# Performance work log

Measured on AMD Instinct MI355X. Metric: run time of the kernel, lower is better.

Reference implementation:

```python
import jax, jax.numpy as jnp
import numpy as np

B, S, N, E = 16, 2048, 256, 4096      # batch, tokens, max entities, edges per sample
H, LD, ETR = 512, 16, 768             # hidden_size, label_emb_dim, transformer dim
D = H + LD                            # graph_dim = 528
C1 = 3                                # num_edge_classes + 1
GL = 2                                # gcn_layers
NLBL = 15                             # num_node_classes + 2


def setup_inputs() -> dict:
    key = jax.random.key(0)
    ks = jax.random.split(key, 14)
    s = 0.02
    inp = {}
    inp["emb"] = jax.random.normal(ks[0], (B, S, ETR), jnp.float32)
    inp["ent_indices"] = jax.random.randint(ks[1], (B, S), 0, N + 1)
    inp["ent_labels"] = jax.random.randint(ks[2], (B, N), 0, NLBL)
    inp["edge_index"] = jax.random.randint(ks[3], (B, 2, E), 0, N + 1)
    inp["edge_attr"] = jax.random.randint(ks[4], (B, E), 0, C1)
    inp["cands"] = jax.random.randint(ks[5], (B, N + 1, N + 1), 0, 2).astype(bool)
    inp["W_red"] = jax.random.normal(ks[6], (ETR, H), jnp.float32) * s
    inp["b_red"] = jnp.zeros((H,), jnp.float32)
    inp["emb_label_tbl"] = jax.random.normal(ks[7], (NLBL, LD), jnp.float32) * s
    inp["W_gcn"] = jax.random.normal(ks[8], (C1, GL, D, D), jnp.float32) * s
    inp["b_gcn"] = jnp.zeros((C1, GL, D), jnp.float32)
    inp["W_head"] = jax.random.normal(ks[9], (D, D), jnp.float32) * s
    inp["b_head"] = jnp.zeros((D,), jnp.float32)
    inp["W_tail"] = jax.random.normal(ks[10], (D, D), jnp.float32) * s
    inp["b_tail"] = jnp.zeros((D,), jnp.float32)
    inp["W_out"] = jax.random.normal(ks[11], (D, C1), jnp.float32) * s
    inp["b_out"] = jnp.zeros((C1,), jnp.float32)
    return inp


def _gcn_layer(x, src, dst, w_e, W, b):
    """PyG GCNConv with edge weights w_e (0/1 relation mask) and self loops.
    x: [n, D]; src/dst: [E]; aggregation flow source->target."""
    n = x.shape[0]
    h = x @ W
    deg = jax.ops.segment_sum(w_e, dst, num_segments=n) + 1.0  # +1 self loop
    dinv = jax.lax.rsqrt(deg)
    coef = w_e * dinv[src] * dinv[dst]                         # D^-1/2 A D^-1/2
    agg = jax.ops.segment_sum(coef[:, None] * h[src], dst, num_segments=n)
    return agg + h / deg[:, None] + b                          # self-loop norm = 1/deg


def reference(emb, ent_indices, ent_labels, edge_index, edge_attr, cands,
              W_red, b_red, emb_label_tbl, W_gcn, b_gcn,
              W_head, b_head, W_tail, b_tail, W_out, b_out):
    n_nodes = cands.shape[1]  # max_num_ent + 1
    # fc_reduction of frozen transformer embeddings
    red = emb @ W_red + b_red                                   # [B,S,H]
    # tag-based segment aggregation: max over (mask * emb) == max(segment_max, 0)
    seg_max = jax.vmap(lambda e, ids: jax.ops.segment_max(e, ids, num_segments=n_nodes))(red, ent_indices)
    ent_hidden = jnp.maximum(seg_max, 0.0).at[:, 0, :].set(0.0)  # tag 0 stays zero
    # label embeddings: tag t uses ent_labels[:, t-1]; zeroed where label==0
    lab = emb_label_tbl[ent_labels] * (ent_labels != 0)[..., None].astype(red.dtype)
    lab0 = jnp.broadcast_to(emb_label_tbl[0], (lab.shape[0], 1, lab.shape[-1]))
    label_part = jnp.concatenate([lab0, lab], axis=1)           # [B,n_nodes,LD]
    x0 = jnp.concatenate([label_part, ent_hidden], axis=-1)     # [B,n_nodes,D]
    # multi-relation GCN: per edge class, stacked GCNConv, summed then averaged
    src, dst = edge_index[:, 0], edge_index[:, 1]
    layer_v = jax.vmap(_gcn_layer, in_axes=(0, 0, 0, 0, None, None))
    result = jnp.zeros_like(x0)
    n_cls = W_gcn.shape[0]
    for c in range(n_cls):
        w_e = (edge_attr == c).astype(x0.dtype)
        x = x0
        for l in range(W_gcn.shape[1]):
            x = layer_v(x, src, dst, w_e, W_gcn[c, l], b_gcn[c, l])
        result = result + x
    result = result / n_cls
    # head/tail projections and 'add' pairwise features gated by candidate mask
    x_head = result @ W_head + b_head
    x_tail = result @ W_tail + b_tail
    m = cands[:, :, 1:].astype(x0.dtype)                        # [B,n_nodes,n_nodes-1]
    # fc_out is linear: ((h_i + t_j) * m_ij) @ W + b == m_ij*(hW_i + tW_j) + b
    hW = x_head @ W_out                                         # [B,n_nodes,C1]
    tW = x_tail[:, 1:] @ W_out                                  # [B,n_nodes-1,C1]
    logits = (hW[:, :, None, :] + tW[:, None, :, :]) * m[..., None] + b_out
    return logits  # [B, n_nodes, n_nodes-1, C1] edge-class logits
```

## Files before the change

kernel.cpp:

```cpp
#include <hip/hip_runtime.h>
#include <hip/hip_bf16.h>

typedef unsigned short u16;
typedef __attribute__((ext_vector_type(8))) short short8;
typedef __attribute__((ext_vector_type(4))) float floatx4;

#define B_ 16
#define S_ 2048
#define NNODE 257
#define E_ 4096
#define ETR_ 768
#define H_ 512
#define D_ 528
#define KPAD 544
#define NC 3
#define NROW (B_*NNODE)
#define DD (D_*D_)

#define BM 128
#define BN 128
#define BK 32

__device__ inline u16 f2b(float x) {
    __hip_bfloat16 h = __float2bfloat16(x);
    return *(u16*)&h;
}
__device__ inline float b2f(u16 u) {
    return __uint_as_float(((unsigned)u) << 16);
}

__device__ inline void gll16(const u16* g, u16* l) {
    __builtin_amdgcn_global_load_lds(
        (const __attribute__((address_space(1))) void*)g,
        (__attribute__((address_space(3))) void*)l,
        16, 0, 0);
}

__device__ inline int clampi(int v, int hi) { return v < hi ? v : hi; }

__global__ void cvt_bf16(const float* __restrict__ in, u16* __restrict__ out, int n4)
{
    const int i = blockIdx.x * 256 + threadIdx.x;
    if (i < n4) {
        const float4 f = ((const float4*)in)[i];
        ushort4 o;
        o.x = f2b(f.x); o.y = f2b(f.y); o.z = f2b(f.z); o.w = f2b(f.w);
        ((ushort4*)out)[i] = o;
    }
}

__global__ void transpose_cvt(const float* __restrict__ in, u16* __restrict__ out,
                              int R, int Cc, size_t instride, size_t outstride,
                              int opitch)
{
    __shared__ float t[32][33];
    const int z = blockIdx.z;
    const int tx = threadIdx.x & 31, ty = threadIdx.x >> 5;
    const int c0 = blockIdx.x * 32, r0 = blockIdx.y * 32;
    const float* ip = in + z * instride;
    u16* op = out + z * outstride;
#pragma unroll
    for (int i = 0; i < 4; i++) {
        const int r = r0 + ty + i * 8, c = c0 + tx;
        if (r < R && c < Cc) t[ty + i * 8][tx] = ip[(size_t)r * Cc + c];
    }
    __syncthreads();
#pragma unroll
    for (int i = 0; i < 4; i++) {
        const int c = c0 + ty + i * 8, r = r0 + tx;
        if (c < Cc && r < R) op[(size_t)c * opitch + r] = f2b(t[tx][ty + i * 8]);
    }
}

template<int SWZ, int OB16>
__global__ __launch_bounds__(256)
void gemm_mfma(const u16* __restrict__ A, const u16* __restrict__ Wt,
               const float* __restrict__ bias_base, size_t bias_stride,
               void* __restrict__ Cv, int M, int N, int K, float scale,
               size_t astride, size_t wstride, size_t cstride, int cpitch)
{
    __shared__ u16 SS[8192];
    const int tid = threadIdx.x;
    const int wave = tid >> 6, lane = tid & 63;
    const int quad = lane >> 4, l16 = lane & 15;
    const int z = blockIdx.z;
    int bx = blockIdx.x, by = blockIdx.y;
    if (SWZ) {
        const int lin = blockIdx.x + (blockIdx.y << 2);
        bx = (lin >> 3) & 3;
        by = (lin & 7) + ((lin >> 5) << 3);
    }
    const int m0 = by * BM, n0 = bx * BN;

    floatx4 acc[2][8];
#pragma unroll
    for (int t = 0; t < 2; t++)
#pragma unroll
        for (int u = 0; u < 8; u++)
#pragma unroll
            for (int r = 0; r < 4; r++) acc[t][u][r] = 0.f;

    const int srow = tid >> 2;
    const int scol = (((tid & 3) ^ ((srow >> 1) & 3))) * 8;
    const u16* aP0 = A + z * astride + (size_t)clampi(m0 + srow,      M - 1) * K + scol;
    const u16* aP1 = A + z * astride + (size_t)clampi(m0 + 64 + srow, M - 1) * K + scol;
    const u16* bP0 = Wt + z * wstride + (size_t)clampi(n0 + srow,      N - 1) * K + scol;
    const u16* bP1 = Wt + z * wstride + (size_t)clampi(n0 + 64 + srow, N - 1) * K + scol;
    u16* const ls = &SS[0] + wave * 512;

    const int sw8 = ((l16 >> 1) & 3) * 8;

    for (int k0 = 0; k0 < K; k0 += BK) {
        gll16(aP0 + k0, ls);
        gll16(aP1 + k0, ls + 2048);
        gll16(bP0 + k0, ls + 4096);
        gll16(bP1 + k0, ls + 6144);
        __syncthreads();
        short8 af[2], bfv[8];
        af[0] = *(const short8*)&SS[(wave * 32 + l16) * 32 + ((quad * 8) ^ sw8)];
        af[1] = *(const short8*)&SS[(wave * 32 + 16 + l16) * 32 + ((quad * 8) ^ sw8)];
#pragma unroll
        for (int u = 0; u < 8; u++)
            bfv[u] = *(const short8*)&SS[4096 + (u * 16 + l16) * 32 + ((quad * 8) ^ sw8)];
#pragma unroll
        for (int t = 0; t < 2; t++)
#pragma unroll
            for (int u = 0; u < 8; u++)
                acc[t][u] = __builtin_amdgcn_mfma_f32_16x16x32_bf16(af[t], bfv[u], acc[t][u], 0, 0, 0);
        __syncthreads();
    }

    const float* bias = bias_base ? (bias_base + z * bias_stride) : nullptr;
#pragma unroll
    for (int t = 0; t < 2; t++) {
#pragma unroll
        for (int r = 0; r < 4; r++) {
            const int m = m0 + wave * 32 + t * 16 + quad * 4 + r;
            if (m >= M) continue;
#pragma unroll
            for (int u = 0; u < 8; u++) {
                const int n = n0 + u * 16 + l16;
                if (n < N) {
                    const float v = acc[t][u][r] * scale + (bias ? bias[n] : 0.f);
                    if (OB16) {
                        u16* Cb = (u16*)Cv;
                        Cb[z * cstride + (size_t)m * cpitch + n] = f2b(v);
                    } else {
                        float* Cf = (float*)Cv;
                        Cf[z * cstride + (size_t)m * cpitch + n] = v;
                    }
                }
            }
        }
    }
}

template<int MODE>
__global__ __launch_bounds__(256)
void gemm64(const float* __restrict__ A, const float* __restrict__ W,
            const float* __restrict__ bias, float* __restrict__ C,
            int M, int N, int K, float scale,
            const int* __restrict__ segidx, float* __restrict__ segout)
{
    __shared__ float Asl[16][68];
    __shared__ float Bsl[16][64];
    const int tid = threadIdx.x;
    const int tx = tid & 15, ty = tid >> 4;
    const int m0 = blockIdx.y * 64, n0 = blockIdx.x * 64;
    const int arow = tid >> 2, acol = (tid & 3) * 4;
    const int brow = tid >> 4, bcol = (tid & 15) * 4;

    float acc[4][4];
#pragma unroll
    for (int i = 0; i < 4; i++)
#pragma unroll
        for (int j = 0; j < 4; j++) acc[i][j] = 0.f;

    for (int kk = 0; kk < K; kk += 16) {
        float4 av = make_float4(0.f, 0.f, 0.f, 0.f);
        if (m0 + arow < M) av = *(const float4*)(A + (size_t)(m0 + arow) * K + kk + acol);
        Asl[acol + 0][arow] = av.x; Asl[acol + 1][arow] = av.y;
        Asl[acol + 2][arow] = av.z; Asl[acol + 3][arow] = av.w;
        float4 bv = make_float4(0.f, 0.f, 0.f, 0.f);
        if (n0 + bcol < N) bv = *(const float4*)(W + (size_t)(kk + brow) * N + n0 + bcol);
        *(float4*)&Bsl[brow][bcol] = bv;
        __syncthreads();
#pragma unroll
        for (int k = 0; k < 16; k++) {
            const float4 a = *(const float4*)&Asl[k][ty * 4];
            const float4 b = *(const float4*)&Bsl[k][tx * 4];
            const float af[4] = { a.x, a.y, a.z, a.w };
            const float bfv[4] = { b.x, b.y, b.z, b.w };
#pragma unroll
            for (int i = 0; i < 4; i++)
#pragma unroll
                for (int j = 0; j < 4; j++) acc[i][j] += af[i] * bfv[j];
        }
        __syncthreads();
    }

#pragma unroll
    for (int i = 0; i < 4; i++) {
        const int m = m0 + ty * 4 + i;
        if (m >= M) continue;
        if (MODE == 1) {
            const int bb = m >> 11;
            const int idx = segidx[m];
            float* const srow = segout + (((size_t)bb * NNODE + idx) << 9);
#pragma unroll
            for (int j = 0; j < 4; j++) {
                const int n = n0 + tx * 4 + j;
                const float v = acc[i][j] + (bias ? bias[n] : 0.f);
                atomicMax(((int*)srow) + n, __float_as_int(v));
            }
        } else {
#pragma unroll
            for (int j = 0; j < 4; j++) {
                const int n = n0 + tx * 4 + j;
                if (n < N) {
                    const float v = acc[i][j] * scale + (bias ? bias[n] : 0.f);
                    C[(size_t)m * N + n] = v;
                }
            }
        }
    }
}

__global__ void csr_all(const int* __restrict__ ent_indices,
                        int* __restrict__ rptr, int* __restrict__ rlist,
                        const int* __restrict__ edge_index, const int* __restrict__ edge_attr,
                        float* __restrict__ degf, int* __restrict__ csr_ptr,
                        int2* __restrict__ csr_sc)
{
    __shared__ int cnt[NC * NNODE];
    __shared__ float dinvl[NC * NNODE];
    const int b = blockIdx.x;
    const int tid = threadIdx.x;

    const int* idx = ent_indices + (size_t)b * S_;
    for (int i = tid; i < NNODE; i += 256) cnt[i] = 0;
    __syncthreads();
    for (int r = tid; r < S_; r += 256) atomicAdd(&cnt[idx[r]], 1);
    __syncthreads();
    if (tid == 0) {
        int run = 0;
        for (int i = 0; i < NNODE; i++) { const int c = cnt[i]; cnt[i] = run; run += c; }
    }
    __syncthreads();
    for (int i = tid; i < NNODE; i += 256) rptr[b * (NNODE + 1) + i] = cnt[i];
    if (tid == 0) rptr[b * (NNODE + 1) + NNODE] = S_;
    __syncthreads();
    for (int r = tid; r < S_; r += 256) {
        const int pos = atomicAdd(&cnt[idx[r]], 1);
        rlist[(size_t)b * S_ + pos] = r;
    }
    __syncthreads();

    const int* src = edge_index + (size_t)b * 2 * E_;
    const int* dst = src + E_;
    const int* attr = edge_attr + (size_t)b * E_;
    for (int i = tid; i < NC * NNODE; i += 256) cnt[i] = 0;
    __syncthreads();
    for (int e = tid; e < E_; e += 256) atomicAdd(&cnt[attr[e] * NNODE + dst[e]], 1);
    __syncthreads();
    for (int i = tid; i < NC * NNODE; i += 256) {
        const float d = (float)cnt[i] + 1.0f;
        degf[(size_t)b * NC * NNODE + i] = d;
        dinvl[i] = rsqrtf(d);
    }
    __syncthreads();
    if (tid == 0) {
        int run = 0;
        for (int i = 0; i < NC * NNODE; i++) { const int c = cnt[i]; cnt[i] = run; run += c; }
    }
    __syncthreads();
    for (int i = tid; i < NC * NNODE; i += 256) csr_ptr[(size_t)b * NC * NNODE + i] = cnt[i];
    __syncthreads();
    for (int e = tid; e < E_; e += 256) {
        const int a = attr[e], d = dst[e], s = src[e];
        const int pos = atomicAdd(&cnt[a * NNODE + d], 1);
        const float cf = dinvl[a * NNODE + s] * dinvl[a * NNODE + d];
        csr_sc[(size_t)b * E_ + pos] = make_int2(s, __float_as_int(cf));
    }
}

__global__ __launch_bounds__(256)
void segmax_x0(const u16* __restrict__ redC, const int* __restrict__ rptr,
               const int* __restrict__ rlist, const float* __restrict__ b_red,
               const int* __restrict__ ent_labels, const float* __restrict__ tbl,
               u16* __restrict__ x0b)
{
    const int bn = blockIdx.x;
    const int b = bn / NNODE, n = bn % NNODE;
    const int tid = threadIdx.x;
    const int c0 = tid * 2;
    const int start = rptr[b * (NNODE + 1) + n];
    const int end   = (n == 0) ? start : rptr[b * (NNODE + 1) + n + 1];
    float m0 = -INFINITY, m1 = -INFINITY;
    const int* rl = rlist + (size_t)b * S_;
    for (int i = start; i < end; i++) {
        const u16* row = redC + ((size_t)b * S_ + rl[i]) * H_;
        const unsigned v = *(const unsigned*)(row + c0);
        m0 = fmaxf(m0, __uint_as_float((v & 0xffffu) << 16));
        m1 = fmaxf(m1, __uint_as_float(v & 0xffff0000u));
    }
    float h0, h1;
    if (n == 0) { h0 = 0.f; h1 = 0.f; }
    else {
        h0 = fmaxf(m0 + b_red[c0], 0.f);
        h1 = fmaxf(m1 + b_red[c0 + 1], 0.f);
    }
    u16* orow = x0b + (size_t)bn * KPAD;
    *(unsigned*)(orow + 16 + c0) = (unsigned)f2b(h0) | ((unsigned)f2b(h1) << 16);
    if (tid < 16) {
        float v;
        if (n == 0) v = tbl[tid];
        else {
            const int lab = ent_labels[b * (NNODE - 1) + (n - 1)];
            v = (lab != 0) ? tbl[lab * 16 + tid] : 0.f;
        }
        orow[tid] = f2b(v);
    } else if (tid < 32) {
        orow[512 + tid] = 0;
    }
}

template<int OUTB>
__global__ void build_x0(const float* __restrict__ seg, const int* __restrict__ ent_labels,
                         const float* __restrict__ tbl, float* __restrict__ x0f,
                         u16* __restrict__ x0b)
{
    const int bn = blockIdx.x;
    const int b = bn / NNODE, n = bn % NNODE;
    const int CMAX = OUTB ? KPAD : D_;
    for (int col = threadIdx.x; col < CMAX; col += blockDim.x) {
        float v;
        if (col >= D_) {
            v = 0.f;
        } else if (col < 16) {
            if (n == 0) v = tbl[col];
            else {
                const int lab = ent_labels[b * (NNODE - 1) + (n - 1)];
                v = (lab != 0) ? tbl[lab * 16 + col] : 0.f;
            }
        } else {
            v = (n == 0) ? 0.f : seg[(((size_t)b * NNODE + n) << 9) + (col - 16)];
        }
        if (OUTB) x0b[(size_t)bn * KPAD + col] = f2b(v);
        else      x0f[(size_t)bn * D_ + col] = v;
    }
}

template<int OUT>
__global__ __launch_bounds__(256)
void gcn_gather(const float* __restrict__ h, size_t hstride,
                const float* __restrict__ degf,
                const int* __restrict__ csr_ptr, const int2* __restrict__ csr_sc,
                const float* __restrict__ bias_base, size_t bias_stride,
                float* __restrict__ outf, u16* __restrict__ outb, size_t ostride,
                int cls0)
{
    const int bn = blockIdx.x;
    const int cls = cls0 + blockIdx.y;
    const int b = bn / NNODE, n = bn % NNODE;
    const int tid = threadIdx.x;
    const int base = b * NC * NNODE + cls * NNODE + n;
    const float d = degf[base];
    const int start = csr_ptr[base];
    const int cnt = (int)d - 1;
    const float inv = 1.0f / d;
    const float* hp = h + blockIdx.y * hstride;
    const float* bias = bias_base + cls * bias_stride;
    const float* hrow = hp + (size_t)bn * D_;
    const int c0 = tid, c1 = tid + 256, c2 = tid + 512;
    float a0 = hrow[c0] * inv + bias[c0];
    float a1 = hrow[c1] * inv + bias[c1];
    float a2 = (c2 < D_) ? hrow[c2] * inv + bias[c2] : 0.f;
    const int2* scp = csr_sc + (size_t)b * E_ + start;
    int2 sc = (cnt > 0) ? scp[0] : make_int2(0, 0);
    for (int i = 0; i < cnt; i++) {
        const int2 cur = sc;
        if (i + 1 < cnt) sc = scp[i + 1];
        const float cf = __int_as_float(cur.y);
        const float* hs = hp + ((size_t)b * NNODE + cur.x) * D_;
        a0 += cf * hs[c0];
        a1 += cf * hs[c1];
        if (c2 < D_) a2 += cf * hs[c2];
    }
    if (OUT == 0) {
        u16* orow = outb + blockIdx.y * ostride + (size_t)bn * KPAD;
        orow[c0] = f2b(a0); orow[c1] = f2b(a1); if (c2 < D_) orow[c2] = f2b(a2);
        if (tid >= 16 && tid < 32) orow[512 + tid] = 0;
    } else if (OUT == 1) {
        float* orow = outf + (size_t)bn * D_;
        orow[c0] += a0; orow[c1] += a1; if (c2 < D_) orow[c2] += a2;
    } else {
        float* orow = outf + blockIdx.y * ostride + (size_t)bn * D_;
        orow[c0] = a0; orow[c1] = a1; if (c2 < D_) orow[c2] = a2;
    }
}

__global__ void rowdot3(const float* __restrict__ x, const float* __restrict__ w,
                        float* __restrict__ out)
{
    const int row = blockIdx.x;
    const int lane = threadIdx.x;
    float a0 = 0.f, a1 = 0.f, a2 = 0.f;
    for (int d = lane; d < D_; d += 64) {
        const float xv = x[(size_t)row * D_ + d];
        a0 += xv * w[d * 3 + 0];
        a1 += xv * w[d * 3 + 1];
        a2 += xv * w[d * 3 + 2];
    }
#pragma unroll
    for (int off = 32; off > 0; off >>= 1) {
        a0 += __shfl_down(a0, off, 64);
        a1 += __shfl_down(a1, off, 64);
        a2 += __shfl_down(a2, off, 64);
    }
    if (lane == 0) {
        out[(size_t)row * 3 + 0] = a0;
        out[(size_t)row * 3 + 1] = a1;
        out[(size_t)row * 3 + 2] = a2;
    }
}

__global__ void prep_heads(const float* __restrict__ W_head, const float* __restrict__ W_tail,
                           const float* __restrict__ b_head, const float* __restrict__ b_tail,
                           const float* __restrict__ W_out,
                           float* __restrict__ Whw, float* __restrict__ Wtw,
                           float* __restrict__ bias6)
{
    const int r = blockIdx.x;
    const int lane = threadIdx.x;
    const float* x; float* o;
    if (r < D_)            { x = W_head + (size_t)r * D_;        o = Whw + (size_t)r * 3; }
    else if (r < 2 * D_)   { x = W_tail + (size_t)(r - D_) * D_; o = Wtw + (size_t)(r - D_) * 3; }
    else if (r == 2 * D_)  { x = b_head;                         o = bias6; }
    else                   { x = b_tail;                         o = bias6 + 3; }
    float a0 = 0.f, a1 = 0.f, a2 = 0.f;
    for (int d = lane; d < D_; d += 64) {
        const float xv = x[d];
        a0 += xv * W_out[d * 3 + 0];
        a1 += xv * W_out[d * 3 + 1];
        a2 += xv * W_out[d * 3 + 2];
    }
#pragma unroll
    for (int off = 32; off > 0; off >>= 1) {
        a0 += __shfl_down(a0, off, 64);
        a1 += __shfl_down(a1, off, 64);
        a2 += __shfl_down(a2, off, 64);
    }
    if (lane == 0) { o[0] = a0; o[1] = a1; o[2] = a2; }
}

__global__ __launch_bounds__(256)
void rowdot6(const float* __restrict__ x3, size_t zstride,
             const float* __restrict__ Whw, const float* __restrict__ Wtw,
             const float* __restrict__ bias6,
             float* __restrict__ hw, float* __restrict__ tw)
{
    const int row = blockIdx.x * 4 + (threadIdx.x >> 6);
    const int lane = threadIdx.x & 63;
    const float* p0 = x3 + (size_t)row * D_;
    const float* p1 = p0 + zstride;
    const float* p2 = p1 + zstride;
    float h0 = 0.f, h1 = 0.f, h2 = 0.f, t0 = 0.f, t1 = 0.f, t2 = 0.f;
    for (int d = lane; d < D_; d += 64) {
        const float xv = (p0[d] + p1[d] + p2[d]) * (1.f / 3.f);
        h0 += xv * Whw[d * 3 + 0]; h1 += xv * Whw[d * 3 + 1]; h2 += xv * Whw[d * 3 + 2];
        t0 += xv * Wtw[d * 3 + 0]; t1 += xv * Wtw[d * 3 + 1]; t2 += xv * Wtw[d * 3 + 2];
    }
#pragma unroll
    for (int off = 32; off > 0; off >>= 1) {
        h0 += __shfl_down(h0, off, 64); h1 += __shfl_down(h1, off, 64); h2 += __shfl_down(h2, off, 64);
        t0 += __shfl_down(t0, off, 64); t1 += __shfl_down(t1, off, 64); t2 += __shfl_down(t2, off, 64);
    }
    if (lane == 0) {
        hw[(size_t)row * 3 + 0] = h0 + bias6[0];
        hw[(size_t)row * 3 + 1] = h1 + bias6[1];
        hw[(size_t)row * 3 + 2] = h2 + bias6[2];
        tw[(size_t)row * 3 + 0] = t0 + bias6[3];
        tw[(size_t)row * 3 + 1] = t1 + bias6[4];
        tw[(size_t)row * 3 + 2] = t2 + bias6[5];
    }
}

__global__ __launch_bounds__(256)
void final_logits(const float* __restrict__ hw, const float* __restrict__ tw,
                  const int* __restrict__ cands, const float* __restrict__ b_out,
                  float* __restrict__ out)
{
    const int bi = blockIdx.x;
    const int b = bi / NNODE;
    const int j = threadIdx.x;
    const float h0 = hw[bi * 3 + 0], h1 = hw[bi * 3 + 1], h2 = hw[bi * 3 + 2];
    const int tj = b * NNODE + 1 + j;
    const float t0 = tw[tj * 3 + 0], t1 = tw[tj * 3 + 1], t2 = tw[tj * 3 + 2];
    const float m = (cands[(size_t)bi * NNODE + 1 + j] != 0) ? 1.f : 0.f;
    const float bo0 = b_out[0], bo1 = b_out[1], bo2 = b_out[2];
    const size_t o = ((size_t)bi * 256 + j) * 3;
    out[o + 0] = (h0 + t0) * m + bo0;
    out[o + 1] = (h1 + t1) * m + bo1;
    out[o + 2] = (h2 + t2) * m + bo2;
}

extern "C" void kernel_launch(void* const* d_in, const int* in_sizes, int n_in,
                              void* d_out, int out_size, void* d_ws, size_t ws_size,
                              hipStream_t stream)
{
    const float* emb       = (const float*)d_in[0];
    const int* ent_indices = (const int*)d_in[1];
    const int* ent_labels  = (const int*)d_in[2];
    const int* edge_index  = (const int*)d_in[3];
    const int* edge_attr   = (const int*)d_in[4];
    const int* cands       = (const int*)d_in[5];
    const float* W_red     = (const float*)d_in[6];
    const float* b_red     = (const float*)d_in[7];
    const float* tbl       = (const float*)d_in[8];
    const float* W_gcn     = (const float*)d_in[9];
    const float* b_gcn     = (const float*)d_in[10];
    const float* W_head    = (const float*)d_in[11];
    const float* b_head    = (const float*)d_in[12];
    const float* W_tail    = (const float*)d_in[13];
    const float* b_tail    = (const float*)d_in[14];
    const float* W_out     = (const float*)d_in[15];
    const float* b_out     = (const float*)d_in[16];

    char* ws = (char*)d_ws;
    size_t off = 0;
    auto alloc = [&](size_t nbytes) -> char* {
        char* p = ws + off; off = (off + nbytes + 255) & ~(size_t)255; return p;
    };
    const size_t ROWB  = (size_t)NROW * D_ * sizeof(float);
    const size_t RD    = (size_t)NROW * D_;
    const size_t RD2   = (size_t)NROW * KPAD;
    const size_t WGZ   = (size_t)2 * D_ * KPAD;

    char* R0      = alloc((size_t)B_ * S_ * ETR_ * sizeof(u16));
    u16*  emb_bf  = (u16*)R0;
    float* hbuf   = (float*)R0;
    u16*  x1b     = (u16*)(R0 + 3 * ROWB);
    char* R1      = alloc((size_t)B_ * S_ * H_ * sizeof(u16));
    u16*  redC    = (u16*)R1;
    float* result3 = (float*)R1;
    int*  rptr    = (int*)alloc((size_t)B_ * (NNODE + 1) * 4);
    int*  rlist   = (int*)alloc((size_t)B_ * S_ * 4);
    u16*  x0b     = (u16*)alloc((size_t)NROW * KPAD * sizeof(u16));
    u16*  wredT   = (u16*)alloc((size_t)H_ * ETR_ * sizeof(u16));
    u16*  wgcnT   = (u16*)alloc((size_t)NC * WGZ * sizeof(u16));
    float* Whw    = (float*)alloc((size_t)D_ * 3 * 4);
    float* Wtw    = (float*)alloc((size_t)D_ * 3 * 4);
    float* bias6  = (float*)alloc(6 * 4);
    float* degf   = (float*)alloc((size_t)B_ * NC * NNODE * 4);
    float* hwp    = (float*)alloc((size_t)NROW * 3 * 4);
    float* twp    = (float*)alloc((size_t)NROW * 3 * 4);
    int* csr_ptr  = (int*)alloc((size_t)B_ * NC * NNODE * 4);
    int2* csr_sc  = (int2*)alloc((size_t)B_ * E_ * 8);
    const bool fast = (ws_size >= off);

    if (fast) {
        const int n4e = (B_ * S_ * ETR_) / 4;
        cvt_bf16<<<(n4e + 255) / 256, 256, 0, stream>>>(emb, emb_bf, n4e);
        transpose_cvt<<<dim3(16, 24, 1), 256, 0, stream>>>(W_red, wredT, ETR_, H_, 0, 0, ETR_);
        hipMemsetAsync(wgcnT, 0, (size_t)NC * WGZ * sizeof(u16), stream);
        transpose_cvt<<<dim3(17, 17, 6), 256, 0, stream>>>(W_gcn, wgcnT, D_, D_, DD, (size_t)D_ * KPAD, KPAD);

        prep_heads<<<2 * D_ + 2, 64, 0, stream>>>(W_head, W_tail, b_head, b_tail, W_out,
                                                  Whw, Wtw, bias6);

        csr_all<<<B_, 256, 0, stream>>>(ent_indices, rptr, rlist,
                                        edge_index, edge_attr, degf, csr_ptr, csr_sc);

        gemm_mfma<1, 1><<<dim3(H_ / BN, (B_ * S_) / BM, 1), 256, 0, stream>>>(
            emb_bf, wredT, nullptr, 0, redC, B_ * S_, H_, ETR_, 1.f, 0, 0, 0, H_);
        segmax_x0<<<B_ * NNODE, 256, 0, stream>>>(redC, rptr, rlist, b_red,
                                                  ent_labels, tbl, x0b);

        dim3 gmm((D_ + BN - 1) / BN, (NROW + BM - 1) / BM, NC);
        gemm_mfma<0, 0><<<gmm, 256, 0, stream>>>(
            x0b, wgcnT, nullptr, 0, hbuf, NROW, D_, KPAD, 1.f, 0, WGZ, RD, D_);
        gcn_gather<0><<<dim3(NROW, NC), 256, 0, stream>>>(
            hbuf, RD, degf, csr_ptr, csr_sc, b_gcn, (size_t)2 * D_,
            nullptr, x1b, RD2, 0);
        gemm_mfma<0, 0><<<gmm, 256, 0, stream>>>(
            x1b, wgcnT + (size_t)D_ * KPAD, nullptr, 0, hbuf, NROW, D_, KPAD, 1.f,
            RD2, WGZ, RD, D_);
        gcn_gather<2><<<dim3(NROW, NC), 256, 0, stream>>>(
            hbuf, RD, degf, csr_ptr, csr_sc, b_gcn + D_, (size_t)2 * D_,
            result3, nullptr, RD, 0);

        rowdot6<<<NROW / 4, 256, 0, stream>>>(result3, RD, Whw, Wtw, bias6, hwp, twp);
        final_logits<<<NROW, 256, 0, stream>>>(hwp, twp, cands, b_out, (float*)d_out);
        return;
    }

    off = 0;
    float* bufA = (float*)alloc(ROWB);
    float* bufB = (float*)alloc(ROWB);
    float* bufC = (float*)alloc(ROWB);
    float* bufD = (float*)alloc(ROWB);
    degf = (float*)alloc((size_t)B_ * NC * NNODE * 4);
    hwp  = (float*)alloc((size_t)NROW * 3 * 4);
    twp  = (float*)alloc((size_t)NROW * 3 * 4);
    csr_ptr = (int*)alloc((size_t)B_ * NC * NNODE * 4);
    csr_sc  = (int2*)alloc((size_t)B_ * E_ * 8);
    int* rptr2  = (int*)alloc((size_t)B_ * (NNODE + 1) * 4);
    int* rlist2 = (int*)alloc((size_t)B_ * S_ * 4);

    hipMemsetAsync(bufA, 0, (size_t)B_ * NNODE * H_ * 4, stream);
    hipMemsetAsync(bufD, 0, ROWB, stream);
    gemm64<1><<<dim3(H_ / 64, (B_ * S_) / 64), 256, 0, stream>>>(
        emb, W_red, b_red, nullptr, B_ * S_, H_, ETR_, 1.f, ent_indices, bufA);
    build_x0<0><<<NROW, 256, 0, stream>>>(bufA, ent_labels, tbl, bufB, nullptr);
    csr_all<<<B_, 256, 0, stream>>>(ent_indices, rptr2, rlist2,
                                    edge_index, edge_attr, degf, csr_ptr, csr_sc);
    dim3 gridG((D_ + 63) / 64, (NROW + 63) / 64);
    for (int c = 0; c < NC; c++) {
        gemm64<0><<<gridG, 256, 0, stream>>>(bufB, W_gcn + (size_t)(c * 2 + 0) * DD,
            nullptr, bufA, NROW, D_, D_, 1.f, nullptr, nullptr);
        gcn_gather<2><<<dim3(NROW, 1), 256, 0, stream>>>(bufA, 0, degf, csr_ptr, csr_sc,
            b_gcn, (size_t)2 * D_, bufC, nullptr, 0, c);
        gemm64<0><<<gridG, 256, 0, stream>>>(bufC, W_gcn + (size_t)(c * 2 + 1) * DD,
            nullptr, bufA, NROW, D_, D_, 1.f, nullptr, nullptr);
        gcn_gather<1><<<dim3(NROW, 1), 256, 0, stream>>>(bufA, 0, degf, csr_ptr, csr_sc,
            b_gcn + D_, (size_t)2 * D_, bufD, nullptr, 0, c);
    }
    gemm64<0><<<gridG, 256, 0, stream>>>(bufD, W_head, b_head, bufB,
        NROW, D_, D_, 1.f / 3.f, nullptr, nullptr);
    gemm64<0><<<gridG, 256, 0, stream>>>(bufD, W_tail, b_tail, bufC,
        NROW, D_, D_, 1.f / 3.f, nullptr, nullptr);
    rowdot3<<<NROW, 64, 0, stream>>>(bufB, W_out, hwp);
    rowdot3<<<NROW, 64, 0, stream>>>(bufC, W_out, twp);
    final_logits<<<NROW, 256, 0, stream>>>(hwp, twp, cands, b_out, (float*)d_out);
}
```

Before: 432.9 us.

## Double-buffer LDS tiles in MFMA GEMM to overlap loads with compute

Doubles the shared-memory tile buffer and prefetches the next K-slice with direct global-to-LDS loads while MFMAs run on the current slice. This drops one of the two barriers per K iteration and is meant to hide global load latency. It doubles LDS use to 32 KB per block, which may lower occupancy. It also assumes K is a multiple of BK, because the tile count is now computed with integer division.

```diff
diff --git a/kernel.cpp b/kernel.cpp
--- a/kernel.cpp
+++ b/kernel.cpp
@@ -79,7 +79,7 @@
                void* __restrict__ Cv, int M, int N, int K, float scale,
                size_t astride, size_t wstride, size_t cstride, int cpitch)
 {
-    __shared__ u16 SS[8192];
+    __shared__ u16 SS[16384];
     const int tid = threadIdx.x;
     const int wave = tid >> 6, lane = tid & 63;
     const int quad = lane >> 4, l16 = lane & 15;
@@ -106,28 +106,44 @@
     const u16* aP1 = A + z * astride + (size_t)clampi(m0 + 64 + srow, M - 1) * K + scol;
     const u16* bP0 = Wt + z * wstride + (size_t)clampi(n0 + srow,      N - 1) * K + scol;
     const u16* bP1 = Wt + z * wstride + (size_t)clampi(n0 + 64 + srow, N - 1) * K + scol;
-    u16* const ls = &SS[0] + wave * 512;
+    const int lsw = wave * 512;
 
     const int sw8 = ((l16 >> 1) & 3) * 8;
 
-    for (int k0 = 0; k0 < K; k0 += BK) {
-        gll16(aP0 + k0, ls);
-        gll16(aP1 + k0, ls + 2048);
-        gll16(bP0 + k0, ls + 4096);
-        gll16(bP1 + k0, ls + 6144);
+    {
+        u16* d = &SS[lsw];
+        gll16(aP0, d);
+        gll16(aP1, d + 2048);
+        gll16(bP0, d + 4096);
+        gll16(bP1, d + 6144);
+    }
+    __syncthreads();
+
+    const int nt = K / BK;
+    int cur = 0;
+    for (int t = 0; t < nt; ++t) {
+        if (t + 1 < nt) {
+            const int kn = (t + 1) * BK;
+            u16* d = &SS[(cur ^ 1) * 8192 + lsw];
+            gll16(aP0 + kn, d);
+            gll16(aP1 + kn, d + 2048);
+            gll16(bP0 + kn, d + 4096);
+            gll16(bP1 + kn, d + 6144);
+        }
+        const u16* Sb = &SS[cur * 8192];
+        short8 af[2], bfv[8];
+        af[0] = *(const short8*)&Sb[(wave * 32 + l16) * 32 + ((quad * 8) ^ sw8)];
+        af[1] = *(const short8*)&Sb[(wave * 32 + 16 + l16) * 32 + ((quad * 8) ^ sw8)];
+#pragma unroll
+        for (int u = 0; u < 8; u++)
+            bfv[u] = *(const short8*)&Sb[4096 + (u * 16 + l16) * 32 + ((quad * 8) ^ sw8)];
+#pragma unroll
+        for (int t2 = 0; t2 < 2; t2++)
+#pragma unroll
+            for (int u = 0; u < 8; u++)
+                acc[t2][u] = __builtin_amdgcn_mfma_f32_16x16x32_bf16(af[t2], bfv[u], acc[t2][u], 0, 0, 0);
         __syncthreads();
-        short8 af[2], bfv[8];
-        af[0] = *(const short8*)&SS[(wave * 32 + l16) * 32 + ((quad * 8) ^ sw8)];
-        af[1] = *(const short8*)&SS[(wave * 32 + 16 + l16) * 32 + ((quad * 8) ^ sw8)];
-#pragma unroll
-        for (int u = 0; u < 8; u++)
-            bfv[u] = *(const short8*)&SS[4096 + (u * 16 + l16) * 32 + ((quad * 8) ^ sw8)];
-#pragma unroll
-        for (int t = 0; t < 2; t++)
-#pragma unroll
-            for (int u = 0; u < 8; u++)
-                acc[t][u] = __builtin_amdgcn_mfma_f32_16x16x32_bf16(af[t], bfv[u], acc[t][u], 0, 0, 0);
-        __syncthreads();
+        cur ^= 1;
     }
 
     const float* bias = bias_base ? (bias_base + z * bias_stride) : nullptr;
```

Result: faster. 423.2 us (-2.2%).
